# Kernel optimization log

Hardware: AMD Instinct MI355X
Metric: run time of the kernel (lower is better)

Reference implementation:

```python
import jax, jax.numpy as jnp
import numpy as np

P = 512       # person_attrs_dim
Z = 4096      # num_zones
T = 16384     # number of timesteps
E = 65536     # number of edges
PENALTY = 10.0


def setup_inputs() -> dict:
    key = jax.random.key(0)
    ks = jax.random.split(key, 10)
    person_attrs = jax.random.normal(ks[0], (P,), dtype=jnp.float32)
    times = jax.random.uniform(ks[1], (T,), dtype=jnp.float32)
    zone_features = jax.random.normal(ks[2], (Z, 16), dtype=jnp.float32)
    edge_index = jax.random.randint(ks[3], (2, E), 0, Z, dtype=jnp.int64)
    s = 0.05
    W1 = jax.random.normal(ks[4], (P + 1, 128), dtype=jnp.float32) * s
    b1 = jnp.zeros((128,), jnp.float32)
    W2 = jax.random.normal(ks[5], (128, 64), dtype=jnp.float32) * s
    b2 = jnp.zeros((64,), jnp.float32)
    W3 = jax.random.normal(ks[6], (64, Z), dtype=jnp.float32) * s
    b3 = jnp.zeros((Z,), jnp.float32)
    return {
        "person_attrs": person_attrs, "times": times,
        "zone_features": zone_features, "edge_index": edge_index,
        "W1": W1, "b1": b1, "W2": W2, "b2": b2, "W3": W3, "b3": b3,
    }


def reference(person_attrs, times, zone_features, edge_index, W1, b1, W2, b2, W3, b3):
    Zn = W3.shape[1]
    Tn = times.shape[0]

    # ---- set_graph_data: symmetric adjacency + self loops ----
    adj = jnp.zeros((Zn, Zn), jnp.float32)
    adj = adj.at[edge_index[0], edge_index[1]].set(1.0)
    adj = adj.at[edge_index[1], edge_index[0]].set(1.0)
    diag = jnp.arange(Zn)
    adj = adj.at[diag, diag].set(1.0)

    # ---- batched MLP over all timesteps (inputs don't depend on decode state) ----
    # input per step: concat(person_attrs, time)  -> [T, P+1]
    x = jnp.concatenate(
        [jnp.broadcast_to(person_attrs, (Tn, person_attrs.shape[0])), times[:, None]],
        axis=1,
    )
    h = jax.nn.relu(x @ W1 + b1)          # [T, 128]  (dropout is identity in eval)
    h = jax.nn.relu(h @ W2 + b2)          # [T, 64]
    raw = h @ W3 + b3                     # [T, Z]

    # ---- sequential graph-masked decode (training=True soft-penalty branch) ----
    def step(cur_zone, raw_t):
        constrained = raw_t - PENALTY * (1.0 - adj[cur_zone])  # [Z]
        nxt = jnp.argmax(constrained).astype(jnp.int32)
        return nxt, constrained

    _, zone_logits = jax.lax.scan(step, jnp.int32(0), raw)     # [T, Z]
    return zone_logits
```

## Files before the change

kernel.cpp:

```cpp
#include <hip/hip_runtime.h>
#include <hip/hip_bf16.h>
#include <stdint.h>

typedef uint16_t u16;
typedef uint32_t u32;
typedef uint64_t u64;
typedef unsigned char u8;

#define TT 16384
#define ZZ 4096
#define EE 65536
#define LBLK 32
#define NBLK 512
#define SUPW 16
#define NSUP 32
#define ADJ_STRIDE 80
#define UCAP 2048
#define PEN 10.0f

#define WS_BITS   0x000000
#define WS_GMKEY  0x200000
#define WS_DEG    0x220000
#define WS_ADJL   0x224000
#define WS_NCH    0x2C4000
#define WS_CVEC   0x2C5000
#define WS_WVEC   0x2C5200
#define WS_H2     0x2C5400
#define WS_M      WS_H2
#define WS_H      0x6C5400
#define WS_SB     0x705400

__device__ __forceinline__ u32 sfu(float v) {
  u32 u = __float_as_uint(v);
  return u ^ ((u32)((int)u >> 31) | 0x80000000u);
}
__device__ __forceinline__ u64 mkkey(float v, u32 z) {
  return ((u64)sfu(v) << 12) | (u64)(4095u - z);
}
__device__ __forceinline__ float key_val(u64 k) {
  u32 sf = (u32)(k >> 12);
  u32 u = (sf & 0x80000000u) ? (sf ^ 0x80000000u) : ~sf;
  return __uint_as_float(u);
}

__device__ __forceinline__ u64 eval_part(int s, int part, const u32* keys, u64 gkey,
                                         const u16* adjl, int nc) {
  const u64* alq = (const u64*)(adjl + (size_t)s * ADJ_STRIDE);
  u64 c0 = (part      < nc) ? alq[part]      : 0;
  u64 c1 = (part + 4  < nc) ? alq[part + 4]  : 0;
  u64 c2 = (part + 8  < nc) ? alq[part + 8]  : 0;
  u64 c3 = (part + 12 < nc) ? alq[part + 12] : 0;
  u64 c4 = (part + 16 < nc) ? alq[part + 16] : 0;
  u64 bb = gkey;
#define CM(cv, cnd) if (cnd) {                                                   \
    u32 lo = (u32)(cv), hi = (u32)((cv) >> 32);                                  \
    u32 za = lo & 0xFFFFu, zb = lo >> 16, zc = hi & 0xFFFFu, zd = hi >> 16;      \
    u64 k0 = ((u64)keys[za] << 32) | (u64)(za ^ 0xFFFu);                         \
    u64 k1 = ((u64)keys[zb] << 32) | (u64)(zb ^ 0xFFFu);                         \
    u64 k2 = ((u64)keys[zc] << 32) | (u64)(zc ^ 0xFFFu);                         \
    u64 k3 = ((u64)keys[zd] << 32) | (u64)(zd ^ 0xFFFu);                         \
    u64 t01 = k0 > k1 ? k0 : k1; u64 t23 = k2 > k3 ? k2 : k3;                    \
    u64 tm = t01 > t23 ? t01 : t23;                                              \
    bb = tm > bb ? tm : bb; }
  CM(c0, part < nc) CM(c1, part + 4 < nc) CM(c2, part + 8 < nc)
  CM(c3, part + 12 < nc) CM(c4, part + 16 < nc)
#undef CM
  return bb;
}

__global__ __launch_bounds__(256) void k_setupA(u32* bits, u32* deg, u16* adjl,
                                                const float* pa, const float* W1,
                                                const float* b1,
                                                float* cvec, float* wvec) {
  __shared__ float pal[512];
  int tid = threadIdx.x;
  if (blockIdx.x < 16) {
    int z = blockIdx.x * 256 + tid;
    bits[(size_t)z * 128 + (z >> 5)] = 1u << (z & 31);
    deg[z] = 1;
    adjl[(size_t)z * ADJ_STRIDE] = (u16)z;
    return;
  }
  for (int i = tid; i < 512; i += 256) pal[i] = pa[i];
  __syncthreads();
  if (tid < 128) {
    float acc = b1[tid];
    for (int i = 0; i < 512; i++) acc = fmaf(pal[i], W1[(size_t)i * 128 + tid], acc);
    cvec[tid] = acc;
    wvec[tid] = W1[512 * 128 + tid];
  }
}

__global__ void k_edges(const int* ei, u32* bits, u32* deg, u16* adjl) {
  int e = blockIdx.x * blockDim.x + threadIdx.x;
  if (e >= EE) return;
  int u = ei[e], v = ei[EE + e];
#pragma unroll
  for (int dir = 0; dir < 2; dir++) {
    int a = dir ? v : u, b = dir ? u : v;
    u32 bit = 1u << (b & 31);
    u32 old = atomicOr(&bits[(size_t)a * 128 + (b >> 5)], bit);
    if (!(old & bit)) {
      u32 p = atomicAdd(&deg[a], 1u);
      if (p < ADJ_STRIDE) adjl[(size_t)a * ADJ_STRIDE + p] = (u16)b;
    }
  }
}

__global__ __launch_bounds__(256) void k_setupC(const u32* deg, u16* adjl, u8* nchp,
                                                const float* times, const float* W2,
                                                const float* b2, const float* cvec,
                                                const float* wvec, float* h2) {
  __shared__ float W2T[64][132];
  __shared__ float h1b[4][128];
  __shared__ float cl[128], wl[128], b2l[64];
  int tid = threadIdx.x;
  if (blockIdx.x < 16) {
    int z = blockIdx.x * 256 + tid;
    int d = (int)deg[z]; if (d > ADJ_STRIDE) d = ADJ_STRIDE;
    int dp = (d + 3) & ~3;
    for (int k = d; k < dp; k++) adjl[(size_t)z * ADJ_STRIDE + k] = (u16)z;
    nchp[z] = (u8)(dp >> 2);
    return;
  }
  for (int idx = tid; idx < 128 * 64; idx += 256) {
    int i = idx >> 6, j = idx & 63;
    W2T[j][i] = W2[idx];
  }
  if (tid < 128) { cl[tid] = cvec[tid]; wl[tid] = wvec[tid]; }
  else if (tid < 192) b2l[tid - 128] = b2[tid - 128];
  __syncthreads();
  int w = tid >> 6, lane = tid & 63;
  int t = (blockIdx.x - 16) * 4 + w;
  float tv = times[t];
  h1b[w][lane]      = fmaxf(fmaf(tv, wl[lane],      cl[lane]),      0.f);
  h1b[w][lane + 64] = fmaxf(fmaf(tv, wl[lane + 64], cl[lane + 64]), 0.f);
  __syncthreads();
  float acc = b2l[lane];
  const float4* hr = (const float4*)&h1b[w][0];
  const float4* Wr = (const float4*)&W2T[lane][0];
#pragma unroll
  for (int i4 = 0; i4 < 32; i4++) {
    float4 a = hr[i4], bb = Wr[i4];
    acc += a.x * bb.x; acc += a.y * bb.y; acc += a.z * bb.z; acc += a.w * bb.w;
  }
  acc = fmaxf(acc, 0.f);
  h2[(size_t)t * 64 + lane] = acc;
}

__global__ __launch_bounds__(256) void k_raw(const float* h2, const float* W3,
                                             const float* b3, float* out,
                                             u64* gmkey) {
  __shared__ float w3t[64][128];
  __shared__ float h2t[64][72];
  int tid = threadIdx.x;
  int zblk = blockIdx.x & 31, tblk = blockIdx.x >> 5;
  int z0 = zblk * 128, t0 = tblk * 64;
#pragma unroll
  for (int it = 0; it < 8; it++) {
    int f4 = tid + it * 256;
    int k = f4 >> 5, jj = (f4 & 31) * 4;
    *(float4*)&w3t[k][jj] = *(const float4*)(W3 + (size_t)k * ZZ + z0 + jj);
  }
#pragma unroll
  for (int it = 0; it < 4; it++) {
    int f4 = tid + it * 256;
    int r = f4 >> 4, kk = (f4 & 15) * 4;
    float4 h = *(const float4*)(h2 + (size_t)(t0 + r) * 64 + kk);
    h2t[kk + 0][r] = h.x; h2t[kk + 1][r] = h.y;
    h2t[kk + 2][r] = h.z; h2t[kk + 3][r] = h.w;
  }
  __syncthreads();
  int zq = tid & 31, tq = tid >> 5;
  float4 acc[8];
#pragma unroll
  for (int r = 0; r < 8; r++) acc[r] = make_float4(0.f, 0.f, 0.f, 0.f);
  for (int k = 0; k < 64; k++) {
    float4 w = *(const float4*)&w3t[k][zq * 4];
    float4 hA = *(const float4*)&h2t[k][tq * 8];
    float4 hB = *(const float4*)&h2t[k][tq * 8 + 4];
    acc[0].x += hA.x * w.x; acc[0].y += hA.x * w.y; acc[0].z += hA.x * w.z; acc[0].w += hA.x * w.w;
    acc[1].x += hA.y * w.x; acc[1].y += hA.y * w.y; acc[1].z += hA.y * w.z; acc[1].w += hA.y * w.w;
    acc[2].x += hA.z * w.x; acc[2].y += hA.z * w.y; acc[2].z += hA.z * w.z; acc[2].w += hA.z * w.w;
    acc[3].x += hA.w * w.x; acc[3].y += hA.w * w.y; acc[3].z += hA.w * w.z; acc[3].w += hA.w * w.w;
    acc[4].x += hB.x * w.x; acc[4].y += hB.x * w.y; acc[4].z += hB.x * w.z; acc[4].w += hB.x * w.w;
    acc[5].x += hB.y * w.x; acc[5].y += hB.y * w.y; acc[5].z += hB.y * w.z; acc[5].w += hB.y * w.w;
    acc[6].x += hB.z * w.x; acc[6].y += hB.z * w.y; acc[6].z += hB.z * w.z; acc[6].w += hB.z * w.w;
    acc[7].x += hB.w * w.x; acc[7].y += hB.w * w.y; acc[7].z += hB.w * w.z; acc[7].w += hB.w * w.w;
  }
  int z = z0 + zq * 4;
  float4 b3v = *(const float4*)(b3 + z);
  int lane = tid & 63;
  int half = lane >> 5;
#pragma unroll
  for (int r = 0; r < 8; r++) {
    int t = t0 + tq * 8 + r;
    float4 v;
    v.x = acc[r].x + b3v.x - PEN; v.y = acc[r].y + b3v.y - PEN;
    v.z = acc[r].z + b3v.z - PEN; v.w = acc[r].w + b3v.w - PEN;
    *(float4*)(out + (size_t)t * ZZ + z) = v;
    float lv = v.x; u32 lz = (u32)z;
    if (v.y > lv) { lv = v.y; lz = (u32)(z + 1); }
    if (v.z > lv) { lv = v.z; lz = (u32)(z + 2); }
    if (v.w > lv) { lv = v.w; lz = (u32)(z + 3); }
    float mv = lv;
#pragma unroll
    for (int off = 16; off >= 1; off >>= 1) {
      float o = __shfl_xor(mv, off);
      mv = o > mv ? o : mv;
    }
    u64 msk = __ballot(lv == mv);
    u32 hm = (u32)(msk >> (half * 32));
    int fl = __ffs(hm) - 1 + half * 32;
    u32 zbest = __shfl(lz, fl);
    if ((lane & 31) == 0)
      atomicMax((unsigned long long*)&gmkey[t], (unsigned long long)mkkey(mv, zbest));
  }
}

__global__ __launch_bounds__(512) void k_stage1(const float* raw, const u16* adjl,
                                                const u8* nchp, const u64* gmkey,
                                                u16* M) {
  __shared__ u32 keys[ZZ];
  __shared__ u16 I[ZZ];
  __shared__ u16 ev[ZZ];
  __shared__ u16 U[2][UCAP];
  __shared__ u8  nchl[ZZ];
  __shared__ u32 markw[128];
  __shared__ u32 mcnt2[2];
  __shared__ u64 gmk[LBLK];
  int tid = threadIdx.x;
  int b = blockIdx.x, t0 = b * LBLK;
  *(u64*)&nchl[tid * 8] = *(const u64*)(nchp + tid * 8);
  if (tid < LBLK) gmk[tid] = gmkey[t0 + tid];
  {
    const float4* src = (const float4*)(raw + (size_t)t0 * ZZ);
    float4 r0 = src[tid], r1 = src[tid + 512];
    ((uint4*)keys)[tid]       = make_uint4(sfu(r0.x), sfu(r0.y), sfu(r0.z), sfu(r0.w));
    ((uint4*)keys)[tid + 512] = make_uint4(sfu(r1.x), sfu(r1.y), sfu(r1.z), sfu(r1.w));
  }
  __syncthreads();
  int lane = tid & 63;
  u64 lmask = (((u64)1) << lane) - 1ull;
  int part = tid & 3;
  int m = ZZ, pb = 0;
  bool dense = true;
  for (int i = 0; i < LBLK; i++) {
    int t = t0 + i;
    int tn = t + 1; if (tn > TT - 1) tn = TT - 1;
    const float4* srcn = (const float4*)(raw + (size_t)tn * ZZ);
    float4 p0 = srcn[tid], p1 = srcn[tid + 512];
    if (tid < 128) markw[tid] = 0;
    if (tid == 128) mcnt2[pb ^ 1] = 0;
    u64 gk = gmk[i];
    float gv = key_val(gk) - PEN;
    u64 gkey = ((u64)sfu(gv) << 32) | (u64)(gk & 0xFFFu);
    int m4 = m << 2;
    for (int u = tid; u < m4; u += 512) {
      int s = dense ? (u >> 2) : (int)U[pb][u >> 2];
      u64 pk = eval_part(s, part, keys, gkey, adjl, (int)nchl[s]);
      u64 o1 = __shfl_xor(pk, 1); pk = o1 > pk ? o1 : pk;
      u64 o2 = __shfl_xor(pk, 2); pk = o2 > pk ? o2 : pk;
      if (part == 0) ev[s] = (u16)(4095u - ((u32)pk & 0xFFFu));
    }
    __syncthreads();
    if (i == 0) {
#pragma unroll
      for (int q = 0; q < 8; q++) {
        int j = tid + q * 512;
        I[j] = ev[j];
      }
    } else {
#pragma unroll
      for (int q = 0; q < 8; q++) {
        int j = tid + q * 512;
        I[j] = ev[I[j]];
      }
    }
    for (int u = tid; u < m; u += 512) {
      int s = dense ? u : (int)U[pb][u];
      u32 ns = ev[s];
      u32 wi = ns >> 5, bit = 1u << (ns & 31);
      u32 old = atomicOr(&markw[wi], bit);
      bool isnew = !(old & bit);
      u64 msk = __ballot(isnew ? 1 : 0);
      u32 base = 0;
      if (lane == 0) base = msk ? atomicAdd(&mcnt2[pb ^ 1], (u32)__popcll(msk)) : 0u;
      base = __shfl(base, 0);
      if (isnew) {
        u32 idx = base + (u32)__popcll(msk & lmask);
        if (idx < UCAP) U[pb ^ 1][idx] = (u16)ns;
      }
    }
    ((uint4*)keys)[tid]       = make_uint4(sfu(p0.x), sfu(p0.y), sfu(p0.z), sfu(p0.w));
    ((uint4*)keys)[tid + 512] = make_uint4(sfu(p1.x), sfu(p1.y), sfu(p1.z), sfu(p1.w));
    __syncthreads();
    m = (int)mcnt2[pb ^ 1];
    dense = (m > UCAP);
    if (dense) m = ZZ;
    pb ^= 1;
  }
  {
    u64* md = (u64*)(M + (size_t)b * ZZ);
    md[tid * 2]     = *(const u64*)&I[tid * 8];
    md[tid * 2 + 1] = *(const u64*)&I[tid * 8 + 4];
  }
}

__global__ __launch_bounds__(256) void k_super(const u16* G, u16* H) {
  int g = blockIdx.x, tid = threadIdx.x;
  u32 v[16];
#pragma unroll
  for (int q = 0; q < 16; q++) v[q] = G[(size_t)(g * SUPW) * ZZ + tid + q * 256];
  for (int k = 1; k < SUPW; k++) {
    const u16* Gk = G + (size_t)(g * SUPW + k) * ZZ;
#pragma unroll
    for (int q = 0; q < 16; q++) v[q] = Gk[v[q]];
  }
#pragma unroll
  for (int q = 0; q < 16; q++) H[(size_t)g * ZZ + tid + q * 256] = (u16)v[q];
}

__global__ void k_chase(const u16* G, const u16* H, u32* sb) {
  __shared__ u32 ug[NSUP];
  int tid = threadIdx.x;
  if (tid == 0) {
    u32 s = 0;
    for (int g = 0; g < NSUP; g++) { ug[g] = s; s = H[(size_t)g * ZZ + s]; }
  }
  __syncthreads();
  if (tid < NSUP) {
    u32 s = ug[tid];
    for (int k = 0; k < SUPW; k++) {
      int b = tid * SUPW + k;
      sb[b] = s;
      s = G[(size_t)b * ZZ + s];
    }
  }
}

__global__ __launch_bounds__(64) void k_replay2(float* out, const u16* adjl,
                                                const u8* nchp, const u64* gmkey,
                                                const u32* sb, const u32* bits) {
  __shared__ u32 curl[LBLK];
  int b = blockIdx.x, t0 = b * LBLK;
  int lane = threadIdx.x;
  u32 s = sb[b];
  for (int i = 0; i < LBLK; i++) {
    int t = t0 + i;
    if (lane == 0) curl[i] = s;
    u64 gk = gmkey[t];
    float gv = key_val(gk) - PEN;
    u32 gi = 4095u - (u32)(gk & 0xFFFu);
    int dp = ((int)nchp[s]) << 2;
    const u16* al = adjl + (size_t)s * ADJ_STRIDE;
    const float* r = out + (size_t)t * ZZ;
    float bv = gv; u32 bi = gi;
    if (lane < dp) {
      u32 nb = al[lane]; float v = r[nb];
      if (v > bv || (v == bv && nb < bi)) { bv = v; bi = nb; }
    }
    if (lane + 64 < dp) {
      u32 nb = al[lane + 64]; float v = r[nb];
      if (v > bv || (v == bv && nb < bi)) { bv = v; bi = nb; }
    }
#pragma unroll
    for (int off = 32; off >= 1; off >>= 1) {
      float ov = __shfl_xor(bv, off);
      u32 oi  = __shfl_xor(bi, off);
      if (ov > bv || (ov == bv && oi < bi)) { bv = ov; bi = oi; }
    }
    s = bi;
  }
  __syncthreads();
  for (int i = 0; i < LBLK; i++) {
    int t = t0 + i;
    u32 c = curl[i];
    u64 w = ((const u64*)(bits + (size_t)c * 128))[lane];
    float* p = out + (size_t)t * ZZ + lane * 64;
    while (w) {
      int bp = __ffsll((unsigned long long)w) - 1;
      p[bp] += PEN;
      w &= w - 1;
    }
  }
}

extern "C" void kernel_launch(void* const* d_in, const int* in_sizes, int n_in,
                              void* d_out, int out_size, void* d_ws, size_t ws_size,
                              hipStream_t stream) {
  const float* pa    = (const float*)d_in[0];
  const float* times = (const float*)d_in[1];
  const int*   ei    = (const int*)d_in[3];
  const float* W1    = (const float*)d_in[4];
  const float* b1    = (const float*)d_in[5];
  const float* W2    = (const float*)d_in[6];
  const float* b2    = (const float*)d_in[7];
  const float* W3    = (const float*)d_in[8];
  const float* b3    = (const float*)d_in[9];
  float* out = (float*)d_out;
  char* ws = (char*)d_ws;

  u32* bits = (u32*)(ws + WS_BITS);
  u64* gmkey = (u64*)(ws + WS_GMKEY);
  u32* deg  = (u32*)(ws + WS_DEG);
  u16* adjl = (u16*)(ws + WS_ADJL);
  u8*  nchp = (u8*)(ws + WS_NCH);
  float* cvec = (float*)(ws + WS_CVEC);
  float* wvec = (float*)(ws + WS_WVEC);
  float* h2   = (float*)(ws + WS_H2);
  u16* M = (u16*)(ws + WS_M);
  u16* H = (u16*)(ws + WS_H);
  u32* sb   = (u32*)(ws + WS_SB);

  hipMemsetAsync(ws, 0, 0x220000, stream);
  hipLaunchKernelGGL(k_setupA, dim3(17), dim3(256), 0, stream,
                     bits, deg, adjl, pa, W1, b1, cvec, wvec);
  hipLaunchKernelGGL(k_edges, dim3(EE / 256), dim3(256), 0, stream, ei, bits, deg, adjl);
  hipLaunchKernelGGL(k_setupC, dim3(16 + TT / 4), dim3(256), 0, stream,
                     deg, adjl, nchp, times, W2, b2, cvec, wvec, h2);
  hipLaunchKernelGGL(k_raw, dim3(8192), dim3(256), 0, stream, h2, W3, b3, out, gmkey);
  hipLaunchKernelGGL(k_stage1, dim3(NBLK), dim3(512), 0, stream, out, adjl, nchp, gmkey, M);
  hipLaunchKernelGGL(k_super, dim3(NSUP), dim3(256), 0, stream, M, H);
  hipLaunchKernelGGL(k_chase, dim3(1), dim3(64), 0, stream, M, H, sb);
  hipLaunchKernelGGL(k_replay2, dim3(NBLK), dim3(64), 0, stream, out, adjl, nchp, gmkey, sb, bits);
}
```

Measured before the change: 456.5 us.

## Shrink stage1 shared memory and split penalty fix-up into separate wide kernel

Cuts k_stage1 LDS use by shrinking the U buffer capacity and dropping the shared nchl copy, reading the per-zone chunk count from global memory instead. This is meant to let more blocks fit per CU. Adjacency chunk loads are now unconditional, with the 16-bit indices masked to 12 bits, which removes branches but reads padding entries. The penalty add-back loop moves out of the 512-block, 64-thread replay kernel into a new kernel with 4096 blocks, passing the current zones through a global array. This spreads the scatter over more waves at the cost of one extra launch, and a smaller UCAP risks overflow if the sparse set grows.

```diff
diff --git a/kernel.cpp b/kernel.cpp
--- a/kernel.cpp
+++ b/kernel.cpp
@@ -15,7 +15,7 @@
 #define SUPW 16
 #define NSUP 32
 #define ADJ_STRIDE 80
-#define UCAP 2048
+#define UCAP 1536
 #define PEN 10.0f
 
 #define WS_BITS   0x000000
@@ -29,6 +29,7 @@
 #define WS_M      WS_H2
 #define WS_H      0x6C5400
 #define WS_SB     0x705400
+#define WS_CUR    0x705C00
 
 __device__ __forceinline__ u32 sfu(float v) {
   u32 u = __float_as_uint(v);
@@ -44,17 +45,19 @@
 }
 
 __device__ __forceinline__ u64 eval_part(int s, int part, const u32* keys, u64 gkey,
-                                         const u16* adjl, int nc) {
+                                         const u16* adjl, const u8* nchp) {
   const u64* alq = (const u64*)(adjl + (size_t)s * ADJ_STRIDE);
-  u64 c0 = (part      < nc) ? alq[part]      : 0;
-  u64 c1 = (part + 4  < nc) ? alq[part + 4]  : 0;
-  u64 c2 = (part + 8  < nc) ? alq[part + 8]  : 0;
-  u64 c3 = (part + 12 < nc) ? alq[part + 12] : 0;
-  u64 c4 = (part + 16 < nc) ? alq[part + 16] : 0;
+  int nc = (int)nchp[s];
+  u64 c0 = alq[part];
+  u64 c1 = alq[part + 4];
+  u64 c2 = alq[part + 8];
+  u64 c3 = alq[part + 12];
+  u64 c4 = alq[part + 16];
   u64 bb = gkey;
 #define CM(cv, cnd) if (cnd) {                                                   \
     u32 lo = (u32)(cv), hi = (u32)((cv) >> 32);                                  \
-    u32 za = lo & 0xFFFFu, zb = lo >> 16, zc = hi & 0xFFFFu, zd = hi >> 16;      \
+    u32 za = lo & 0xFFFu, zb = (lo >> 16) & 0xFFFu;                              \
+    u32 zc = hi & 0xFFFu, zd = (hi >> 16) & 0xFFFu;                              \
     u64 k0 = ((u64)keys[za] << 32) | (u64)(za ^ 0xFFFu);                         \
     u64 k1 = ((u64)keys[zb] << 32) | (u64)(zb ^ 0xFFFu);                         \
     u64 k2 = ((u64)keys[zc] << 32) | (u64)(zc ^ 0xFFFu);                         \
@@ -225,13 +228,11 @@
   __shared__ u16 I[ZZ];
   __shared__ u16 ev[ZZ];
   __shared__ u16 U[2][UCAP];
-  __shared__ u8  nchl[ZZ];
   __shared__ u32 markw[128];
   __shared__ u32 mcnt2[2];
   __shared__ u64 gmk[LBLK];
   int tid = threadIdx.x;
   int b = blockIdx.x, t0 = b * LBLK;
-  *(u64*)&nchl[tid * 8] = *(const u64*)(nchp + tid * 8);
   if (tid < LBLK) gmk[tid] = gmkey[t0 + tid];
   {
     const float4* src = (const float4*)(raw + (size_t)t0 * ZZ);
@@ -258,7 +259,7 @@
     int m4 = m << 2;
     for (int u = tid; u < m4; u += 512) {
       int s = dense ? (u >> 2) : (int)U[pb][u >> 2];
-      u64 pk = eval_part(s, part, keys, gkey, adjl, (int)nchl[s]);
+      u64 pk = eval_part(s, part, keys, gkey, adjl, nchp);
       u64 o1 = __shfl_xor(pk, 1); pk = o1 > pk ? o1 : pk;
       u64 o2 = __shfl_xor(pk, 2); pk = o2 > pk ? o2 : pk;
       if (part == 0) ev[s] = (u16)(4095u - ((u32)pk & 0xFFFu));
@@ -339,16 +340,15 @@
   }
 }
 
-__global__ __launch_bounds__(64) void k_replay2(float* out, const u16* adjl,
+__global__ __launch_bounds__(64) void k_replay2(const float* out, const u16* adjl,
                                                 const u8* nchp, const u64* gmkey,
-                                                const u32* sb, const u32* bits) {
-  __shared__ u32 curl[LBLK];
+                                                const u32* sb, u32* curz) {
   int b = blockIdx.x, t0 = b * LBLK;
   int lane = threadIdx.x;
   u32 s = sb[b];
   for (int i = 0; i < LBLK; i++) {
     int t = t0 + i;
-    if (lane == 0) curl[i] = s;
+    if (lane == 0) curz[t] = s;
     u64 gk = gmkey[t];
     float gv = key_val(gk) - PEN;
     u32 gi = 4095u - (u32)(gk & 0xFFFu);
@@ -372,17 +372,18 @@
     }
     s = bi;
   }
-  __syncthreads();
-  for (int i = 0; i < LBLK; i++) {
-    int t = t0 + i;
-    u32 c = curl[i];
-    u64 w = ((const u64*)(bits + (size_t)c * 128))[lane];
-    float* p = out + (size_t)t * ZZ + lane * 64;
-    while (w) {
-      int bp = __ffsll((unsigned long long)w) - 1;
-      p[bp] += PEN;
-      w &= w - 1;
-    }
+}
+
+__global__ __launch_bounds__(256) void k_out2(float* out, const u32* curz, const u32* bits) {
+  int t = blockIdx.x * 4 + (threadIdx.x >> 6);
+  int lane = threadIdx.x & 63;
+  u32 c = curz[t];
+  u64 w = ((const u64*)(bits + (size_t)c * 128))[lane];
+  float* p = out + (size_t)t * ZZ + lane * 64;
+  while (w) {
+    int bpos = __ffsll((unsigned long long)w) - 1;
+    p[bpos] += PEN;
+    w &= w - 1;
   }
 }
 
@@ -412,6 +413,7 @@
   u16* M = (u16*)(ws + WS_M);
   u16* H = (u16*)(ws + WS_H);
   u32* sb   = (u32*)(ws + WS_SB);
+  u32* curz = (u32*)(ws + WS_CUR);
 
   hipMemsetAsync(ws, 0, 0x220000, stream);
   hipLaunchKernelGGL(k_setupA, dim3(17), dim3(256), 0, stream,
@@ -423,5 +425,6 @@
   hipLaunchKernelGGL(k_stage1, dim3(NBLK), dim3(512), 0, stream, out, adjl, nchp, gmkey, M);
   hipLaunchKernelGGL(k_super, dim3(NSUP), dim3(256), 0, stream, M, H);
   hipLaunchKernelGGL(k_chase, dim3(1), dim3(64), 0, stream, M, H, sb);
-  hipLaunchKernelGGL(k_replay2, dim3(NBLK), dim3(64), 0, stream, out, adjl, nchp, gmkey, sb, bits);
-}
+  hipLaunchKernelGGL(k_replay2, dim3(NBLK), dim3(64), 0, stream, out, adjl, nchp, gmkey, sb, curz);
+  hipLaunchKernelGGL(k_out2, dim3(TT / 4), dim3(256), 0, stream, out, curz, bits);
+}
```

After: 440.3 us. -3.6%, faster.
